# Kernel optimization log

Measured on AMD Instinct MI355X. Metric: run time of the kernel, lower is better.

Reference implementation:

```python
import jax, jax.numpy as jnp
import numpy as np
from jax import lax

WINDOW_SIZE = 11
SIGMA = 1.5
C1 = 0.01 ** 2
C2 = 0.03 ** 2


def _create_window(window_size, channel):
    xs = np.arange(window_size)
    g = np.exp(-((xs - window_size // 2) ** 2) / (2.0 * SIGMA ** 2))
    g = (g / g.sum()).astype(np.float32)
    w2d = np.outer(g, g)  # [k, k]
    # depthwise kernel in OIHW with feature_group_count=channel: [channel, 1, k, k]
    return jnp.asarray(np.broadcast_to(w2d, (channel, 1, window_size, window_size)).copy())


def _dw_conv(x, window, pad):
    # x: [B, C, H, W], window: [C, 1, k, k]; depthwise conv, SAME-style padding
    c = x.shape[1]
    return lax.conv_general_dilated(
        x, window,
        window_strides=(1, 1),
        padding=[(pad, pad), (pad, pad)],
        dimension_numbers=('NCHW', 'OIHW', 'NCHW'),
        feature_group_count=c,
    )


def setup_inputs() -> dict:
    key = jax.random.key(0)
    k1, k2 = jax.random.split(key)
    img1 = jax.random.uniform(k1, (32, 1, 512, 512), dtype=jnp.float32)
    img2 = jax.random.uniform(k2, (32, 1, 512, 512), dtype=jnp.float32)
    return {"img1": img1, "img2": img2}


def reference(img1, img2):
    channel = img1.shape[1]
    pad = WINDOW_SIZE // 2
    window = _create_window(WINDOW_SIZE, channel)

    mu1 = _dw_conv(img1, window, pad)
    mu2 = _dw_conv(img2, window, pad)
    mu1_sq = mu1 * mu1
    mu2_sq = mu2 * mu2
    mu1_mu2 = mu1 * mu2

    sigma1_sq = _dw_conv(img1 * img1, window, pad) - mu1_sq
    sigma2_sq = _dw_conv(img2 * img2, window, pad) - mu2_sq
    sigma12 = _dw_conv(img1 * img2, window, pad) - mu1_mu2

    ssim_map = ((2.0 * mu1_mu2 + C1) * (2.0 * sigma12 + C2)) / (
        (mu1_sq + mu2_sq + C1) * (sigma1_sq + sigma2_sq + C2))
    return 1.0 - jnp.mean(ssim_map)
```

## Files before the change

### kernel.cpp

```cpp
#include <hip/hip_runtime.h>

typedef _Float16 f16x8 __attribute__((ext_vector_type(8)));
typedef _Float16 f16x4 __attribute__((ext_vector_type(4)));
typedef __fp16 fp16x2 __attribute__((ext_vector_type(2)));
typedef float f32x4 __attribute__((ext_vector_type(4)));

#define IMG 512
#define NB 32
#define OUTC 118
#define OUTR 32
#define GX 5
#define GY 16
#define NBLK (GX*GY*NB)
#define INSTR 48
#define VSTR 136
#define VOFF (16*VSTR)

#define GW_LIST { 0.0010283804f, 0.0075987583f, 0.0360007700f, 0.1093606900f, \
  0.2130055300f, 0.2660117200f, 0.2130055300f, 0.1093606900f, 0.0360007700f, \
  0.0075987583f, 0.0010283804f }

__global__ __launch_bounds__(256, 3) void ssim_mfma(const float* __restrict__ img1,
                                                    const float* __restrict__ img2,
                                                    float* __restrict__ partials) {
    __shared__ _Float16 lds_in[2][128][INSTR];
    __shared__ _Float16 lds_v[5*VOFF + 32];
    __shared__ _Float16 gwt[64];
    __shared__ float red[4];

    const int tid  = threadIdx.x;
    const int lane = tid & 63;
    const int lm   = lane & 15;
    const int kg   = lane >> 4;
    const int w    = tid >> 6;

    const int bx = blockIdx.x, by = blockIdx.y, bz = blockIdx.z;
    const float* __restrict__ p1 = img1 + (size_t)bz * (IMG*IMG);
    const float* __restrict__ p2 = img2 + (size_t)bz * (IMG*IMG);
    const int x0 = bx * OUTC;
    const int y0 = by * OUTR;

    const int ci = tid & 127;
    const int hh = tid >> 7;
    const int gc = x0 - 5 + ci;
    const bool okc = (gc >= 0) && (gc < IMG);
    const int gcc  = okc ? gc : 0;

    {
        union { fp16x2 p2v[12]; f16x8 v[3]; } ua, ub;
        const int slot0 = hh * 24;
#pragma unroll
        for (int pp = 0; pp < 12; ++pp) {
            const int s0 = slot0 + 2*pp;
            const int ar0 = y0 - 5 + s0;
            const int ar1 = ar0 + 1;
            const bool ok0 = okc & (s0   < 42) & (ar0 >= 0) & (ar0 < IMG);
            const bool ok1 = okc & (s0+1 < 42) & (ar1 >= 0) & (ar1 < IMG);
            const int i0 = ok0 ? ar0 : 0, i1 = ok1 ? ar1 : 0;
            float a0 = p1[i0*IMG + gcc], a1 = p1[i1*IMG + gcc];
            float b0 = p2[i0*IMG + gcc], b1 = p2[i1*IMG + gcc];
            a0 = ok0 ? a0 : 0.f;  a1 = ok1 ? a1 : 0.f;
            b0 = ok0 ? b0 : 0.f;  b1 = ok1 ? b1 : 0.f;
            ua.p2v[pp] = __builtin_amdgcn_cvt_pkrtz(a0, a1);
            ub.p2v[pp] = __builtin_amdgcn_cvt_pkrtz(b0, b1);
        }
#pragma unroll
        for (int m = 0; m < 3; ++m) {
            *(f16x8*)&lds_in[0][ci][slot0 + 8*m] = ua.v[m];
            *(f16x8*)&lds_in[1][ci][slot0 + 8*m] = ub.v[m];
        }
    }
    {
        const float GWc[11] = GW_LIST;
        if (tid < 64) {
            float wv = 0.f;
            const int t = tid - 16;
#pragma unroll
            for (int k = 0; k < 11; ++k) if (t == k) wv = GWc[k];
            gwt[tid] = (_Float16)wv;
        }
        f16x8 z = {};
        if (tid >= 64 && tid < 144) {
            const int u = tid - 64;
            const int f = u / 16, r = u % 16;
            *(f16x8*)&lds_v[f*VOFF + r*VSTR + 128] = z;
        } else if (tid >= 144 && tid < 148) {
            *(f16x8*)&lds_v[5*VOFF + (tid-144)*8] = z;
        }
    }
    __syncthreads();

    union { _Float16 h[8]; f16x8 v; } wu;
#pragma unroll
    for (int i = 0; i < 8; ++i) wu.h[i] = gwt[16 + kg*8 + i - lm];

    float local = 0.f;
    const f32x4 zc = {0.f, 0.f, 0.f, 0.f};

    auto stage_v = [&](int sbase) {
#pragma unroll
        for (int q = 0; q < 2; ++q) {
            const int cb = 2*w + q;
            const f16x8 xf = *(const f16x8*)&lds_in[0][cb*16 + lm][sbase + kg*8];
            const f16x8 yf = *(const f16x8*)&lds_in[1][cb*16 + lm][sbase + kg*8];
            const f16x8 fr0 = xf, fr1 = yf;
            const f16x8 fr2 = xf*xf, fr3 = yf*yf, fr4 = xf*yf;
            const int cbase = cb*16 + kg*4;
#define DO_F(F, FR) { \
            const f32x4 d = __builtin_amdgcn_mfma_f32_16x16x32_f16(FR, wu.v, zc, 0, 0, 0); \
            union { fp16x2 p[2]; f16x4 v4; } pk; \
            pk.p[0] = __builtin_amdgcn_cvt_pkrtz(d[0], d[1]); \
            pk.p[1] = __builtin_amdgcn_cvt_pkrtz(d[2], d[3]); \
            *(f16x4*)&lds_v[(F)*VOFF + lm*VSTR + cbase] = pk.v4; }
            DO_F(0, fr0) DO_F(1, fr1) DO_F(2, fr2) DO_F(3, fr3) DO_F(4, fr4)
#undef DO_F
        }
    };

    auto stage_h = [&]() {
#pragma unroll
        for (int q = 0; q < 2; ++q) {
            const int xx = 2*w + q;
            const int cb2 = xx*16 + kg*8;
            const f16x8 a0 = *(const f16x8*)&lds_v[0*VOFF + lm*VSTR + cb2];
            const f16x8 a1 = *(const f16x8*)&lds_v[1*VOFF + lm*VSTR + cb2];
            const f16x8 a2 = *(const f16x8*)&lds_v[2*VOFF + lm*VSTR + cb2];
            const f16x8 a3 = *(const f16x8*)&lds_v[3*VOFF + lm*VSTR + cb2];
            const f16x8 a4 = *(const f16x8*)&lds_v[4*VOFF + lm*VSTR + cb2];
            const f32x4 d0 = __builtin_amdgcn_mfma_f32_16x16x32_f16(a0, wu.v, zc, 0,0,0);
            const f32x4 d1 = __builtin_amdgcn_mfma_f32_16x16x32_f16(a1, wu.v, zc, 0,0,0);
            const f32x4 d2 = __builtin_amdgcn_mfma_f32_16x16x32_f16(a2, wu.v, zc, 0,0,0);
            const f32x4 d3 = __builtin_amdgcn_mfma_f32_16x16x32_f16(a3, wu.v, zc, 0,0,0);
            const f32x4 d4 = __builtin_amdgcn_mfma_f32_16x16x32_f16(a4, wu.v, zc, 0,0,0);
            const int X = xx*16 + lm;
            const bool valid = (X < OUTC) & (x0 + X < IMG);
            float s4 = 0.f;
#pragma unroll
            for (int j = 0; j < 4; ++j) {
                const float mu1 = d0[j], mu2 = d1[j];
                const float m11 = mu1*mu1, m22 = mu2*mu2, m12 = mu1*mu2;
                const float s1 = d2[j] - m11, s2 = d3[j] - m22, sx = d4[j] - m12;
                const float num = (2.f*m12 + 1e-4f) * (2.f*sx + 9e-4f);
                const float den = (m11 + m22 + 1e-4f) * (s1 + s2 + 9e-4f);
                s4 += num * __builtin_amdgcn_rcpf(den);
            }
            local += valid ? s4 : 0.f;
        }
    };

    stage_v(0);
    __syncthreads();
    stage_h();
    __syncthreads();
    stage_v(16);
    __syncthreads();
    stage_h();

#pragma unroll
    for (int off = 32; off > 0; off >>= 1)
        local += __shfl_down(local, off, 64);
    if (lane == 0) red[w] = local;
    __syncthreads();
    if (tid == 0) {
        partials[(size_t)((bz*GY + by)*GX + bx)] = red[0] + red[1] + red[2] + red[3];
    }
}

__global__ __launch_bounds__(256) void ssim_finalize(const float* __restrict__ partials,
                                                     float* __restrict__ out) {
    __shared__ double red[4];
    double s = 0.0;
    for (int i = threadIdx.x; i < NBLK/4; i += 256) {
        const float4 v = reinterpret_cast<const float4*>(partials)[i];
        s += (double)v.x + (double)v.y + (double)v.z + (double)v.w;
    }
#pragma unroll
    for (int off = 32; off > 0; off >>= 1)
        s += __shfl_down(s, off, 64);
    if ((threadIdx.x & 63) == 0) red[threadIdx.x >> 6] = s;
    __syncthreads();
    if (threadIdx.x == 0) {
        double tot = red[0] + red[1] + red[2] + red[3];
        out[0] = (float)(1.0 - tot / (32.0 * 512.0 * 512.0));
    }
}

extern "C" void kernel_launch(void* const* d_in, const int* in_sizes, int n_in,
                              void* d_out, int out_size, void* d_ws, size_t ws_size,
                              hipStream_t stream) {
    const float* img1 = (const float*)d_in[0];
    const float* img2 = (const float*)d_in[1];
    float* out = (float*)d_out;
    float* partials = (float*)d_ws;

    dim3 grid(GX, GY, NB);
    ssim_mfma<<<grid, 256, 0, stream>>>(img1, img2, partials);
    ssim_finalize<<<1, 256, 0, stream>>>(partials, out);
}
```

Before: 28.42 us.

## Shrink input LDS tile and prefetch second row strip during horizontal pass

New measurement: 29.64 us. 1.04x slower.

```diff
diff --git a/kernel.cpp b/kernel.cpp
--- a/kernel.cpp
+++ b/kernel.cpp
@@ -12,7 +12,7 @@
 #define GX 5
 #define GY 16
 #define NBLK (GX*GY*NB)
-#define INSTR 48
+#define INSTR 32
 #define VSTR 136
 #define VOFF (16*VSTR)
 
@@ -20,7 +20,7 @@
   0.2130055300f, 0.2660117200f, 0.2130055300f, 0.1093606900f, 0.0360007700f, \
   0.0075987583f, 0.0010283804f }
 
-__global__ __launch_bounds__(256, 3) void ssim_mfma(const float* __restrict__ img1,
+__global__ __launch_bounds__(256, 4) void ssim_mfma(const float* __restrict__ img1,
                                                     const float* __restrict__ img2,
                                                     float* __restrict__ partials) {
     __shared__ _Float16 lds_in[2][128][INSTR];
@@ -45,17 +45,18 @@
     const int gc = x0 - 5 + ci;
     const bool okc = (gc >= 0) && (gc < IMG);
     const int gcc  = okc ? gc : 0;
-
-    {
-        union { fp16x2 p2v[12]; f16x8 v[3]; } ua, ub;
-        const int slot0 = hh * 24;
-#pragma unroll
-        for (int pp = 0; pp < 12; ++pp) {
+    const int slot0 = hh * 16;
+
+    typedef union { fp16x2 p2v[8]; f16x8 v[2]; } pack16;
+
+    auto load_strip = [&](int ybase, pack16& ua, pack16& ub) {
+#pragma unroll
+        for (int pp = 0; pp < 8; ++pp) {
             const int s0 = slot0 + 2*pp;
-            const int ar0 = y0 - 5 + s0;
+            const int ar0 = ybase + s0;
             const int ar1 = ar0 + 1;
-            const bool ok0 = okc & (s0   < 42) & (ar0 >= 0) & (ar0 < IMG);
-            const bool ok1 = okc & (s0+1 < 42) & (ar1 >= 0) & (ar1 < IMG);
+            const bool ok0 = okc & (s0   < 26) & (ar0 >= 0) & (ar0 < IMG);
+            const bool ok1 = okc & (s0+1 < 26) & (ar1 >= 0) & (ar1 < IMG);
             const int i0 = ok0 ? ar0 : 0, i1 = ok1 ? ar1 : 0;
             float a0 = p1[i0*IMG + gcc], a1 = p1[i1*IMG + gcc];
             float b0 = p2[i0*IMG + gcc], b1 = p2[i1*IMG + gcc];
@@ -64,11 +65,18 @@
             ua.p2v[pp] = __builtin_amdgcn_cvt_pkrtz(a0, a1);
             ub.p2v[pp] = __builtin_amdgcn_cvt_pkrtz(b0, b1);
         }
-#pragma unroll
-        for (int m = 0; m < 3; ++m) {
-            *(f16x8*)&lds_in[0][ci][slot0 + 8*m] = ua.v[m];
-            *(f16x8*)&lds_in[1][ci][slot0 + 8*m] = ub.v[m];
-        }
+    };
+    auto write_strip = [&](pack16& ua, pack16& ub) {
+        *(f16x8*)&lds_in[0][ci][slot0]     = ua.v[0];
+        *(f16x8*)&lds_in[0][ci][slot0 + 8] = ua.v[1];
+        *(f16x8*)&lds_in[1][ci][slot0]     = ub.v[0];
+        *(f16x8*)&lds_in[1][ci][slot0 + 8] = ub.v[1];
+    };
+
+    {
+        pack16 ua, ub;
+        load_strip(y0 - 5, ua, ub);
+        write_strip(ua, ub);
     }
     {
         const float GWc[11] = GW_LIST;
@@ -97,12 +105,12 @@
     float local = 0.f;
     const f32x4 zc = {0.f, 0.f, 0.f, 0.f};
 
-    auto stage_v = [&](int sbase) {
+    auto stage_v = [&]() {
 #pragma unroll
         for (int q = 0; q < 2; ++q) {
             const int cb = 2*w + q;
-            const f16x8 xf = *(const f16x8*)&lds_in[0][cb*16 + lm][sbase + kg*8];
-            const f16x8 yf = *(const f16x8*)&lds_in[1][cb*16 + lm][sbase + kg*8];
+            const f16x8 xf = *(const f16x8*)&lds_in[0][cb*16 + lm][kg*8];
+            const f16x8 yf = *(const f16x8*)&lds_in[1][cb*16 + lm][kg*8];
             const f16x8 fr0 = xf, fr1 = yf;
             const f16x8 fr2 = xf*xf, fr3 = yf*yf, fr4 = xf*yf;
             const int cbase = cb*16 + kg*4;
@@ -148,11 +156,18 @@
         }
     };
 
-    stage_v(0);
-    __syncthreads();
+    stage_v();
+    __syncthreads();
+
+    pack16 ua1, ub1;
+    load_strip(y0 + 11, ua1, ub1);
+
     stage_h();
-    __syncthreads();
-    stage_v(16);
+
+    write_strip(ua1, ub1);
+    __syncthreads();
+
+    stage_v();
     __syncthreads();
     stage_h();
 
```

## Compute both vertical passes up front and reuse input LDS for second buffer

Applied to the files above, without the earlier changes.

Result: no change. 28.25 us (-0.6%).

```diff
diff --git a/kernel.cpp b/kernel.cpp
--- a/kernel.cpp
+++ b/kernel.cpp
@@ -13,8 +13,11 @@
 #define GY 16
 #define NBLK (GX*GY*NB)
 #define INSTR 48
+#define IOFF (128*INSTR)
 #define VSTR 136
 #define VOFF (16*VSTR)
+#define VLEN (5*VOFF + 32)
+#define BUF0 (2*IOFF)
 
 #define GW_LIST { 0.0010283804f, 0.0075987583f, 0.0360007700f, 0.1093606900f, \
   0.2130055300f, 0.2660117200f, 0.2130055300f, 0.1093606900f, 0.0360007700f, \
@@ -23,8 +26,7 @@
 __global__ __launch_bounds__(256, 3) void ssim_mfma(const float* __restrict__ img1,
                                                     const float* __restrict__ img2,
                                                     float* __restrict__ partials) {
-    __shared__ _Float16 lds_in[2][128][INSTR];
-    __shared__ _Float16 lds_v[5*VOFF + 32];
+    __shared__ _Float16 smem[BUF0 + VLEN];
     __shared__ _Float16 gwt[64];
     __shared__ float red[4];
 
@@ -64,10 +66,11 @@
             ua.p2v[pp] = __builtin_amdgcn_cvt_pkrtz(a0, a1);
             ub.p2v[pp] = __builtin_amdgcn_cvt_pkrtz(b0, b1);
         }
+        _Float16* dst = &smem[ci*INSTR + slot0];
 #pragma unroll
         for (int m = 0; m < 3; ++m) {
-            *(f16x8*)&lds_in[0][ci][slot0 + 8*m] = ua.v[m];
-            *(f16x8*)&lds_in[1][ci][slot0 + 8*m] = ub.v[m];
+            *(f16x8*)(dst + 8*m)        = ua.v[m];
+            *(f16x8*)(dst + IOFF + 8*m) = ub.v[m];
         }
     }
     {
@@ -83,9 +86,9 @@
         if (tid >= 64 && tid < 144) {
             const int u = tid - 64;
             const int f = u / 16, r = u % 16;
-            *(f16x8*)&lds_v[f*VOFF + r*VSTR + 128] = z;
+            *(f16x8*)&smem[BUF0 + f*VOFF + r*VSTR + 128] = z;
         } else if (tid >= 144 && tid < 148) {
-            *(f16x8*)&lds_v[5*VOFF + (tid-144)*8] = z;
+            *(f16x8*)&smem[BUF0 + 5*VOFF + (tid-144)*8] = z;
         }
     }
     __syncthreads();
@@ -94,52 +97,68 @@
 #pragma unroll
     for (int i = 0; i < 8; ++i) wu.h[i] = gwt[16 + kg*8 + i - lm];
 
-    float local = 0.f;
     const f32x4 zc = {0.f, 0.f, 0.f, 0.f};
 
-    auto stage_v = [&](int sbase) {
+    f16x4 pk[2][2][5];
+#pragma unroll
+    for (int s = 0; s < 2; ++s) {
 #pragma unroll
         for (int q = 0; q < 2; ++q) {
             const int cb = 2*w + q;
-            const f16x8 xf = *(const f16x8*)&lds_in[0][cb*16 + lm][sbase + kg*8];
-            const f16x8 yf = *(const f16x8*)&lds_in[1][cb*16 + lm][sbase + kg*8];
-            const f16x8 fr0 = xf, fr1 = yf;
-            const f16x8 fr2 = xf*xf, fr3 = yf*yf, fr4 = xf*yf;
-            const int cbase = cb*16 + kg*4;
-#define DO_F(F, FR) { \
-            const f32x4 d = __builtin_amdgcn_mfma_f32_16x16x32_f16(FR, wu.v, zc, 0, 0, 0); \
-            union { fp16x2 p[2]; f16x4 v4; } pk; \
-            pk.p[0] = __builtin_amdgcn_cvt_pkrtz(d[0], d[1]); \
-            pk.p[1] = __builtin_amdgcn_cvt_pkrtz(d[2], d[3]); \
-            *(f16x4*)&lds_v[(F)*VOFF + lm*VSTR + cbase] = pk.v4; }
-            DO_F(0, fr0) DO_F(1, fr1) DO_F(2, fr2) DO_F(3, fr3) DO_F(4, fr4)
-#undef DO_F
-        }
-    };
-
-    auto stage_h = [&]() {
+            const _Float16* colp = &smem[(cb*16 + lm)*INSTR + s*16 + kg*8];
+            const f16x8 xf = *(const f16x8*)colp;
+            const f16x8 yf = *(const f16x8*)(colp + IOFF);
+            const f16x8 fr[5] = { xf, yf, xf*xf, yf*yf, xf*yf };
+#pragma unroll
+            for (int f = 0; f < 5; ++f) {
+                const f32x4 d = __builtin_amdgcn_mfma_f32_16x16x32_f16(fr[f], wu.v, zc, 0, 0, 0);
+                union { fp16x2 p[2]; f16x4 v4; } c;
+                c.p[0] = __builtin_amdgcn_cvt_pkrtz(d[0], d[1]);
+                c.p[1] = __builtin_amdgcn_cvt_pkrtz(d[2], d[3]);
+                pk[s][q][f] = c.v4;
+            }
+        }
+    }
+
+    {
+        _Float16* b = &smem[BUF0 + lm*VSTR + 2*w*16 + kg*4];
+#pragma unroll
+        for (int q = 0; q < 2; ++q)
+#pragma unroll
+            for (int f = 0; f < 5; ++f)
+                *(f16x4*)(b + f*VOFF + q*16) = pk[0][q][f];
+    }
+    __syncthreads();
+
+    {
+        _Float16* b = &smem[lm*VSTR + 2*w*16 + kg*4];
+#pragma unroll
+        for (int q = 0; q < 2; ++q)
+#pragma unroll
+            for (int f = 0; f < 5; ++f)
+                *(f16x4*)(b + f*VOFF + q*16) = pk[1][q][f];
+    }
+
+    float local = 0.f;
+    auto stage_h = [&](int base) {
 #pragma unroll
         for (int q = 0; q < 2; ++q) {
             const int xx = 2*w + q;
-            const int cb2 = xx*16 + kg*8;
-            const f16x8 a0 = *(const f16x8*)&lds_v[0*VOFF + lm*VSTR + cb2];
-            const f16x8 a1 = *(const f16x8*)&lds_v[1*VOFF + lm*VSTR + cb2];
-            const f16x8 a2 = *(const f16x8*)&lds_v[2*VOFF + lm*VSTR + cb2];
-            const f16x8 a3 = *(const f16x8*)&lds_v[3*VOFF + lm*VSTR + cb2];
-            const f16x8 a4 = *(const f16x8*)&lds_v[4*VOFF + lm*VSTR + cb2];
-            const f32x4 d0 = __builtin_amdgcn_mfma_f32_16x16x32_f16(a0, wu.v, zc, 0,0,0);
-            const f32x4 d1 = __builtin_amdgcn_mfma_f32_16x16x32_f16(a1, wu.v, zc, 0,0,0);
-            const f32x4 d2 = __builtin_amdgcn_mfma_f32_16x16x32_f16(a2, wu.v, zc, 0,0,0);
-            const f32x4 d3 = __builtin_amdgcn_mfma_f32_16x16x32_f16(a3, wu.v, zc, 0,0,0);
-            const f32x4 d4 = __builtin_amdgcn_mfma_f32_16x16x32_f16(a4, wu.v, zc, 0,0,0);
+            const _Float16* vp = &smem[base + lm*VSTR + xx*16 + kg*8];
+            f32x4 d[5];
+#pragma unroll
+            for (int f = 0; f < 5; ++f) {
+                const f16x8 a = *(const f16x8*)(vp + f*VOFF);
+                d[f] = __builtin_amdgcn_mfma_f32_16x16x32_f16(a, wu.v, zc, 0, 0, 0);
+            }
             const int X = xx*16 + lm;
             const bool valid = (X < OUTC) & (x0 + X < IMG);
             float s4 = 0.f;
 #pragma unroll
             for (int j = 0; j < 4; ++j) {
-                const float mu1 = d0[j], mu2 = d1[j];
+                const float mu1 = d[0][j], mu2 = d[1][j];
                 const float m11 = mu1*mu1, m22 = mu2*mu2, m12 = mu1*mu2;
-                const float s1 = d2[j] - m11, s2 = d3[j] - m22, sx = d4[j] - m12;
+                const float s1 = d[2][j] - m11, s2 = d[3][j] - m22, sx = d[4][j] - m12;
                 const float num = (2.f*m12 + 1e-4f) * (2.f*sx + 9e-4f);
                 const float den = (m11 + m22 + 1e-4f) * (s1 + s2 + 9e-4f);
                 s4 += num * __builtin_amdgcn_rcpf(den);
@@ -148,13 +167,9 @@
         }
     };
 
-    stage_v(0);
-    __syncthreads();
-    stage_h();
-    __syncthreads();
-    stage_v(16);
-    __syncthreads();
-    stage_h();
+    stage_h(BUF0);
+    __syncthreads();
+    stage_h(0);
 
 #pragma unroll
     for (int off = 32; off > 0; off >>= 1)
```
